# Optimization experiments

Measured on AMD Instinct MI355X. Metric: run time of the kernel, lower is better.

Reference implementation:

```python
import jax, jax.numpy as jnp
import numpy as np

B, T, D = 128, 197, 768          # batch, tokens, model dim
HEADS, HID_PER_HEAD = 12, 64
H = HEADS * HID_PER_HEAD         # lstm hidden size (== D by construction)


def _block_mask(in_per_head, hid_per_head, head_num):
    """Block-diagonal mask replicated over the 4 LSTM gates (i,f,g,o)."""
    Ht = hid_per_head * head_num
    Dt = in_per_head * head_num
    m = np.zeros((4 * Ht, Dt), np.float32)
    for h in range(head_num):
        for g in range(4):
            r0 = g * Ht + h * hid_per_head
            m[r0:r0 + hid_per_head, h * in_per_head:(h + 1) * in_per_head] = 1.0
    return jnp.asarray(m)


def setup_inputs() -> dict:
    key = jax.random.key(0)
    ks = jax.random.split(key, 16)
    s = 1.0 / np.sqrt(H)  # pytorch LSTM init scale
    u = lambda k, shape: jax.random.uniform(k, shape, jnp.float32, -s, s)
    mask_ih = _block_mask(D // HEADS, HID_PER_HEAD, HEADS)   # [4H, D]
    mask_hh = _block_mask(HID_PER_HEAD, HID_PER_HEAD, HEADS)  # [4H, H]
    inp = {
        "x": jax.random.normal(ks[0], (B, T, D), jnp.float32),
        "pre_w": u(ks[1], (D, D)),
        "pre_b": u(ks[2], (D,)),
        "w_ih_f": u(ks[3], (4 * H, D)) * mask_ih,
        "w_hh_f": u(ks[4], (4 * H, H)) * mask_hh,
        "b_ih_f": u(ks[5], (4 * H,)),
        "b_hh_f": u(ks[6], (4 * H,)),
        "w_ih_r": u(ks[7], (4 * H, D)) * mask_ih,
        "w_hh_r": u(ks[8], (4 * H, H)) * mask_hh,
        "b_ih_r": u(ks[9], (4 * H,)),
        "b_hh_r": u(ks[10], (4 * H,)),
        "proj_w": u(ks[11], (D, 2 * H)),
        "proj_b": u(ks[12], (D,)),
    }
    return inp


def _lstm_dir(x, w_ih, w_hh, b_ih, b_hh, reverse):
    # Precompute input contribution for all timesteps: [B,T,4H]
    xg = jnp.einsum('btd,gd->btg', x, w_ih) + b_ih + b_hh
    xs = jnp.swapaxes(xg, 0, 1)  # [T,B,4H]
    Bn = x.shape[0]

    def step(carry, gx):
        h, c = carry
        gates = gx + h @ w_hh.T
        i, f, g, o = jnp.split(gates, 4, axis=-1)  # pytorch gate order i,f,g,o
        i = jax.nn.sigmoid(i)
        f = jax.nn.sigmoid(f)
        g = jnp.tanh(g)
        o = jax.nn.sigmoid(o)
        c = f * c + i * g
        h = o * jnp.tanh(c)
        return (h, c), h

    init = (jnp.zeros((Bn, w_hh.shape[1]), x.dtype),
            jnp.zeros((Bn, w_hh.shape[1]), x.dtype))
    _, hs = jax.lax.scan(step, init, xs, reverse=reverse)  # outputs aligned to input order
    return jnp.swapaxes(hs, 0, 1)  # [B,T,H]


def reference(x, pre_w, pre_b, w_ih_f, w_hh_f, b_ih_f, b_hh_f,
              w_ih_r, w_hh_r, b_ih_r, b_hh_r, proj_w, proj_b):
    x = x @ pre_w.T + pre_b                      # pre_proj
    hf = _lstm_dir(x, w_ih_f, w_hh_f, b_ih_f, b_hh_f, reverse=False)
    hr = _lstm_dir(x, w_ih_r, w_hh_r, b_ih_r, b_hh_r, reverse=True)
    lstm_out = jnp.concatenate([hf, hr], axis=-1)  # [B,T,2H]
    return lstm_out @ proj_w.T + proj_b            # proj -> [B,T,D]
```

## Files before the change

kernel.cpp:

```cpp
#include <hip/hip_runtime.h>
#include <stdint.h>

#define DEV __device__ __forceinline__

typedef __attribute__((ext_vector_type(8))) short short8;
typedef __attribute__((ext_vector_type(4))) float floatx4;

#define BATCH 128
#define TT    197
#define DD    768
#define NH    12
#define NROWS (BATCH*TT)
#define G4H   3072

DEV uint16_t f2bf(float f) {
    union { float f; uint32_t u; } v; v.f = f;
    uint32_t r = (v.u + 0x7FFF + ((v.u >> 16) & 1)) >> 16;
    return (uint16_t)r;
}

DEV floatx4 mfma16(short8 a, short8 b, floatx4 c) {
    return __builtin_amdgcn_mfma_f32_16x16x32_bf16(a, b, c, 0, 0, 0);
}

DEV float sigf(float x)   { return __builtin_amdgcn_rcpf(1.0f + __expf(-x)); }
DEV float tanhf_(float x) { return 1.0f - 2.0f * __builtin_amdgcn_rcpf(1.0f + __expf(2.0f * x)); }

DEV void async16(const uint16_t* g, uint16_t* l) {
    __builtin_amdgcn_global_load_lds(
        (const __attribute__((address_space(1))) unsigned int*)g,
        (__attribute__((address_space(3))) unsigned int*)l,
        16, 0, 0);
}

__global__ void cvt_bf16(const float* __restrict__ src, uint16_t* __restrict__ dst, int n4) {
    int i = blockIdx.x * blockDim.x + threadIdx.x;
    int stride = gridDim.x * blockDim.x;
    for (; i < n4; i += stride) {
        float4 v = ((const float4*)src)[i];
        ushort4 o;
        o.x = f2bf(v.x); o.y = f2bf(v.y); o.z = f2bf(v.z); o.w = f2bf(v.w);
        ((ushort4*)dst)[i] = o;
    }
}

template<int STORE_BF16, int REMAP>
__global__ __launch_bounds__(256) void gemm128(
    const uint16_t* __restrict__ A,
    const uint16_t* __restrict__ Bw,
    const float*    __restrict__ bias,
    void*           __restrict__ C,
    int K, int Ntot)
{
    __shared__ __attribute__((aligned(16))) uint16_t As[128 * 32];
    __shared__ __attribute__((aligned(16))) uint16_t Bs[128 * 32];

    const int tid  = threadIdx.x;
    const int wv   = tid >> 6;
    const int lane = tid & 63;
    const int ln   = lane & 15;
    const int q    = lane >> 4;
    const int m0   = blockIdx.y * 128;
    const int n0   = blockIdx.x * 128;
    const int wm   = wv >> 1;
    const int wn   = wv & 1;

    floatx4 acc[4][4];
#pragma unroll
    for (int a = 0; a < 4; a++)
#pragma unroll
        for (int b = 0; b < 4; b++) acc[a][b] = (floatx4){0.f, 0.f, 0.f, 0.f};

    const uint16_t* gA0 = A  + (size_t)(m0 + (2*wv+0)*16 + ln) * K + q*8;
    const uint16_t* gA1 = A  + (size_t)(m0 + (2*wv+1)*16 + ln) * K + q*8;
    const uint16_t* gB0 = Bw + (size_t)(n0 + (2*wv+0)*16 + ln) * K + q*8;
    const uint16_t* gB1 = Bw + (size_t)(n0 + (2*wv+1)*16 + ln) * K + q*8;
    uint16_t* lA0 = &As[(2*wv+0) * 512];
    uint16_t* lA1 = &As[(2*wv+1) * 512];
    uint16_t* lB0 = &Bs[(2*wv+0) * 512];
    uint16_t* lB1 = &Bs[(2*wv+1) * 512];

    for (int k0 = 0; k0 < K; k0 += 32) {
        __syncthreads();
        async16(gA0 + k0, lA0);
        async16(gA1 + k0, lA1);
        async16(gB0 + k0, lB0);
        async16(gB1 + k0, lB1);
        __syncthreads();

        short8 af[4], bf[4];
#pragma unroll
        for (int mt = 0; mt < 4; mt++)
            af[mt] = *(const short8*)&As[(wm*4 + mt)*512 + lane*8];
#pragma unroll
        for (int nt = 0; nt < 4; nt++)
            bf[nt] = *(const short8*)&Bs[(wn*4 + nt)*512 + lane*8];
#pragma unroll
        for (int mt = 0; mt < 4; mt++)
#pragma unroll
            for (int nt = 0; nt < 4; nt++)
                acc[mt][nt] = mfma16(af[mt], bf[nt], acc[mt][nt]);
    }

#pragma unroll
    for (int mt = 0; mt < 4; mt++)
#pragma unroll
        for (int nt = 0; nt < 4; nt++) {
            int n = n0 + (wn*4 + nt)*16 + ln;
            float bv = bias[n];
#pragma unroll
            for (int r = 0; r < 4; r++) {
                int m = m0 + (wm*4 + mt)*16 + q*4 + r;
                float val = acc[mt][nt][r] + bv;
                int row;
                if (REMAP) { int b = m / 197; int t = m - b*197; row = t*128 + b; }
                else       { row = m; }
                if (STORE_BF16) ((uint16_t*)C)[(size_t)row * Ntot + n] = f2bf(val);
                else            ((float*)C)[(size_t)row * Ntot + n]    = val;
            }
        }
}

__global__ __launch_bounds__(256) void lstm_fused(
    const uint16_t* __restrict__ pre,
    const uint16_t* __restrict__ wih_f, const uint16_t* __restrict__ whh_f,
    const uint16_t* __restrict__ wih_r, const uint16_t* __restrict__ whh_r,
    const float* __restrict__ bih_f, const float* __restrict__ bhh_f,
    const float* __restrict__ bih_r, const float* __restrict__ bhh_r,
    uint16_t* __restrict__ hout)
{
    __shared__ __attribute__((aligned(16))) uint16_t hbuf[16][72];

    const int tid  = threadIdx.x;
    const int wv   = tid >> 6;
    const int lane = tid & 63;
    const int ln   = lane & 15;
    const int q    = lane >> 4;
    const int b0   = blockIdx.x * 16;
    const int head = blockIdx.y;
    const int dir  = blockIdx.z;
    const int ub   = wv * 16;

    const uint16_t* wih = dir ? wih_r : wih_f;
    const uint16_t* whh = dir ? whh_r : whh_f;
    const float*    bih = dir ? bih_r : bih_f;
    const float*    bhh = dir ? bhh_r : bhh_f;

    short8 aih[4][2], ahh[4][2];
#pragma unroll
    for (int t = 0; t < 4; t++) {
        size_t row = (size_t)(t*768 + head*64 + ub + ln);
#pragma unroll
        for (int s = 0; s < 2; s++) {
            aih[t][s] = *(const short8*)(wih + row*768 + head*64 + s*32 + q*8);
            ahh[t][s] = *(const short8*)(whh + row*768 + head*64 + s*32 + q*8);
        }
    }
    float biasv[4][4];
#pragma unroll
    for (int t = 0; t < 4; t++)
#pragma unroll
        for (int r = 0; r < 4; r++) {
            int row = t*768 + head*64 + ub + q*4 + r;
            biasv[t][r] = bih[row] + bhh[row];
        }

    for (int i = tid; i < 16*72; i += 256) ((uint16_t*)hbuf)[i] = 0;
    float c[4] = {0.f, 0.f, 0.f, 0.f};
    __syncthreads();

    const uint16_t* xbase = pre + head*64 + q*8;
    int t_cur = dir ? (TT - 1) : 0;
    const int tstep = dir ? -1 : 1;
    size_t xo = (size_t)(t_cur*128 + b0 + ln) * 768;
    short8 xv0 = *(const short8*)(xbase + xo);
    short8 xv1 = *(const short8*)(xbase + xo + 32);

    for (int step = 0; step < TT; step++) {
        short8 cx0 = xv0, cx1 = xv1;
        int t_next = t_cur + tstep;
        if (step + 1 < TT) {
            size_t xo2 = (size_t)(t_next*128 + b0 + ln) * 768;
            xv0 = *(const short8*)(xbase + xo2);
            xv1 = *(const short8*)(xbase + xo2 + 32);
        }
        short8 hb0 = *(const short8*)&hbuf[ln][0*32 + q*8];
        short8 hb1 = *(const short8*)&hbuf[ln][1*32 + q*8];

        floatx4 acc[4];
#pragma unroll
        for (int t = 0; t < 4; t++)
            acc[t] = (floatx4){biasv[t][0], biasv[t][1], biasv[t][2], biasv[t][3]};
#pragma unroll
        for (int t = 0; t < 4; t++) {
            acc[t] = mfma16(aih[t][0], cx0, acc[t]);
            acc[t] = mfma16(ahh[t][0], hb0, acc[t]);
            acc[t] = mfma16(aih[t][1], cx1, acc[t]);
            acc[t] = mfma16(ahh[t][1], hb1, acc[t]);
        }

        union { uint16_t s[4]; uint2 v; } hp;
#pragma unroll
        for (int r = 0; r < 4; r++) {
            float ig = sigf(acc[0][r]);
            float fg = sigf(acc[1][r]);
            float gg = tanhf_(acc[2][r]);
            float og = sigf(acc[3][r]);
            c[r] = fg * c[r] + ig * gg;
            float hv = og * tanhf_(c[r]);
            hp.s[r] = f2bf(hv);
        }

        __syncthreads();
        *(uint2*)&hbuf[ln][ub + q*4] = hp.v;
        __syncthreads();

        {
            int bl = tid >> 4;
            int dw = tid & 15;
            uint2 v = *(const uint2*)&hbuf[bl][dw*4];
            size_t off = ((size_t)(b0 + bl)*TT + t_cur) * 1536 + dir*768 + head*64 + dw*4;
            *(uint2*)(hout + off) = v;
        }
        t_cur = t_next;
    }
}

extern "C" void kernel_launch(void* const* d_in, const int* in_sizes, int n_in,
                              void* d_out, int out_size, void* d_ws, size_t ws_size,
                              hipStream_t stream) {
    (void)in_sizes; (void)n_in; (void)out_size; (void)ws_size;
    const float* x     = (const float*)d_in[0];
    const float* pre_w = (const float*)d_in[1];
    const float* pre_b = (const float*)d_in[2];
    const float* wihf  = (const float*)d_in[3];
    const float* whhf  = (const float*)d_in[4];
    const float* bihf  = (const float*)d_in[5];
    const float* bhhf  = (const float*)d_in[6];
    const float* wihr  = (const float*)d_in[7];
    const float* whhr  = (const float*)d_in[8];
    const float* bihr  = (const float*)d_in[9];
    const float* bhhr  = (const float*)d_in[10];
    const float* projw = (const float*)d_in[11];
    const float* projb = (const float*)d_in[12];
    float* out = (float*)d_out;

    uint16_t* W = (uint16_t*)d_ws;
    uint16_t* xb     = W; W += (size_t)NROWS * DD;
    uint16_t* bwpre  = W; W += (size_t)DD * DD;
    uint16_t* bwihf  = W; W += (size_t)G4H * DD;
    uint16_t* bwhhf  = W; W += (size_t)G4H * DD;
    uint16_t* bwihr  = W; W += (size_t)G4H * DD;
    uint16_t* bwhhr  = W; W += (size_t)G4H * DD;
    uint16_t* bwproj = W; W += (size_t)DD * 2 * DD;
    uint16_t* preb   = W; W += (size_t)NROWS * DD;
    uint16_t* houtb  = W; W += (size_t)NROWS * 2 * DD;

    auto cvt = [&](const float* s, uint16_t* d, size_t n) {
        int n4 = (int)(n / 4);
        int blocks = (n4 + 255) / 256; if (blocks > 4096) blocks = 4096;
        hipLaunchKernelGGL(cvt_bf16, dim3(blocks), dim3(256), 0, stream, s, d, n4);
    };
    cvt(x,     xb,     (size_t)NROWS * DD);
    cvt(pre_w, bwpre,  (size_t)DD * DD);
    cvt(wihf,  bwihf,  (size_t)G4H * DD);
    cvt(whhf,  bwhhf,  (size_t)G4H * DD);
    cvt(wihr,  bwihr,  (size_t)G4H * DD);
    cvt(whhr,  bwhhr,  (size_t)G4H * DD);
    cvt(projw, bwproj, (size_t)DD * 2 * DD);

    hipLaunchKernelGGL((gemm128<1, 1>), dim3(6, 197), dim3(256), 0, stream,
                       xb, bwpre, pre_b, (void*)preb, DD, DD);
    hipLaunchKernelGGL(lstm_fused, dim3(8, 12, 2), dim3(256), 0, stream,
                       preb, bwihf, bwhhf, bwihr, bwhhr,
                       bihf, bhhf, bihr, bhhr, houtb);
    hipLaunchKernelGGL((gemm128<0, 0>), dim3(6, 197), dim3(256), 0, stream,
                       houtb, bwproj, projb, (void*)out, 2 * DD, DD);
}
```

Measured before the change: 511.8 us.

## Fuse conversions, double-buffer LSTM h, head-major pre layout, swizzled GEMM grid

Merges the seven fp32-to-bf16 conversion launches into one multi-segment kernel. The GEMMs now load a 64-wide K slice per barrier pair and use a 1D grid with XCD-aware block swizzling. The pre-projection output is written in a [t][head][batch][64] layout so each LSTM step reads contiguous memory. The LSTM hidden state is double-buffered in LDS, which removes one barrier per recurrent step. Together these target launch overhead, barrier count on the serial recurrence and strided loads, at the cost of extra LDS and a more complex index mapping.

```diff
diff --git a/kernel.cpp b/kernel.cpp
--- a/kernel.cpp
+++ b/kernel.cpp
@@ -12,6 +12,8 @@
 #define NH    12
 #define NROWS (BATCH*TT)
 #define G4H   3072
+#define MT    197
+#define NT    6
 
 DEV uint16_t f2bf(float f) {
     union { float f; uint32_t u; } v; v.f = f;
@@ -33,18 +35,30 @@
         16, 0, 0);
 }
 
-__global__ void cvt_bf16(const float* __restrict__ src, uint16_t* __restrict__ dst, int n4) {
-    int i = blockIdx.x * blockDim.x + threadIdx.x;
+struct CvtArgs {
+    const float* src[7];
+    uint16_t*    dst[7];
+    int          n4[7];
+    int          nseg;
+};
+
+__global__ void cvt_multi(CvtArgs a) {
+    int tid = blockIdx.x * blockDim.x + threadIdx.x;
     int stride = gridDim.x * blockDim.x;
-    for (; i < n4; i += stride) {
-        float4 v = ((const float4*)src)[i];
-        ushort4 o;
-        o.x = f2bf(v.x); o.y = f2bf(v.y); o.z = f2bf(v.z); o.w = f2bf(v.w);
-        ((ushort4*)dst)[i] = o;
+    for (int s = 0; s < a.nseg; s++) {
+        const float4* src = (const float4*)a.src[s];
+        ushort4* dst = (ushort4*)a.dst[s];
+        int n4 = a.n4[s];
+        for (int i = tid; i < n4; i += stride) {
+            float4 v = src[i];
+            ushort4 o;
+            o.x = f2bf(v.x); o.y = f2bf(v.y); o.z = f2bf(v.z); o.w = f2bf(v.w);
+            dst[i] = o;
+        }
     }
 }
 
-template<int STORE_BF16, int REMAP>
+template<int STORE_BF16, int LAYOUT>
 __global__ __launch_bounds__(256) void gemm128(
     const uint16_t* __restrict__ A,
     const uint16_t* __restrict__ Bw,
@@ -52,16 +66,23 @@
     void*           __restrict__ C,
     int K, int Ntot)
 {
-    __shared__ __attribute__((aligned(16))) uint16_t As[128 * 32];
-    __shared__ __attribute__((aligned(16))) uint16_t Bs[128 * 32];
+    __shared__ __attribute__((aligned(16))) uint16_t As[2][8 * 512];
+    __shared__ __attribute__((aligned(16))) uint16_t Bs[2][8 * 512];
+
+    const int bid = blockIdx.x;
+    const int c   = bid & 7;
+    const int j   = bid >> 3;
+    const int mt_ = c + 8 * (j / NT);
+    const int nt_ = j % NT;
+    if (mt_ >= MT) return;
+    const int m0 = mt_ * 128;
+    const int n0 = nt_ * 128;
 
     const int tid  = threadIdx.x;
     const int wv   = tid >> 6;
     const int lane = tid & 63;
     const int ln   = lane & 15;
     const int q    = lane >> 4;
-    const int m0   = blockIdx.y * 128;
-    const int n0   = blockIdx.x * 128;
     const int wm   = wv >> 1;
     const int wn   = wv & 1;
 
@@ -75,31 +96,38 @@
     const uint16_t* gA1 = A  + (size_t)(m0 + (2*wv+1)*16 + ln) * K + q*8;
     const uint16_t* gB0 = Bw + (size_t)(n0 + (2*wv+0)*16 + ln) * K + q*8;
     const uint16_t* gB1 = Bw + (size_t)(n0 + (2*wv+1)*16 + ln) * K + q*8;
-    uint16_t* lA0 = &As[(2*wv+0) * 512];
-    uint16_t* lA1 = &As[(2*wv+1) * 512];
-    uint16_t* lB0 = &Bs[(2*wv+0) * 512];
-    uint16_t* lB1 = &Bs[(2*wv+1) * 512];
-
-    for (int k0 = 0; k0 < K; k0 += 32) {
+    uint16_t* lA0h0 = &As[0][(2*wv+0)*512]; uint16_t* lA0h1 = &As[1][(2*wv+0)*512];
+    uint16_t* lA1h0 = &As[0][(2*wv+1)*512]; uint16_t* lA1h1 = &As[1][(2*wv+1)*512];
+    uint16_t* lB0h0 = &Bs[0][(2*wv+0)*512]; uint16_t* lB0h1 = &Bs[1][(2*wv+0)*512];
+    uint16_t* lB1h0 = &Bs[0][(2*wv+1)*512]; uint16_t* lB1h1 = &Bs[1][(2*wv+1)*512];
+
+    for (int k0 = 0; k0 < K; k0 += 64) {
         __syncthreads();
-        async16(gA0 + k0, lA0);
-        async16(gA1 + k0, lA1);
-        async16(gB0 + k0, lB0);
-        async16(gB1 + k0, lB1);
+        async16(gA0 + k0,      lA0h0);
+        async16(gA0 + k0 + 32, lA0h1);
+        async16(gA1 + k0,      lA1h0);
+        async16(gA1 + k0 + 32, lA1h1);
+        async16(gB0 + k0,      lB0h0);
+        async16(gB0 + k0 + 32, lB0h1);
+        async16(gB1 + k0,      lB1h0);
+        async16(gB1 + k0 + 32, lB1h1);
         __syncthreads();
 
-        short8 af[4], bf[4];
-#pragma unroll
-        for (int mt = 0; mt < 4; mt++)
-            af[mt] = *(const short8*)&As[(wm*4 + mt)*512 + lane*8];
-#pragma unroll
-        for (int nt = 0; nt < 4; nt++)
-            bf[nt] = *(const short8*)&Bs[(wn*4 + nt)*512 + lane*8];
-#pragma unroll
-        for (int mt = 0; mt < 4; mt++)
+#pragma unroll
+        for (int h = 0; h < 2; h++) {
+            short8 af[4], bf[4];
+#pragma unroll
+            for (int mt = 0; mt < 4; mt++)
+                af[mt] = *(const short8*)&As[h][(wm*4 + mt)*512 + lane*8];
 #pragma unroll
             for (int nt = 0; nt < 4; nt++)
-                acc[mt][nt] = mfma16(af[mt], bf[nt], acc[mt][nt]);
+                bf[nt] = *(const short8*)&Bs[h][(wn*4 + nt)*512 + lane*8];
+#pragma unroll
+            for (int mt = 0; mt < 4; mt++)
+#pragma unroll
+                for (int nt = 0; nt < 4; nt++)
+                    acc[mt][nt] = mfma16(af[mt], bf[nt], acc[mt][nt]);
+        }
     }
 
 #pragma unroll
@@ -112,11 +140,16 @@
             for (int r = 0; r < 4; r++) {
                 int m = m0 + (wm*4 + mt)*16 + q*4 + r;
                 float val = acc[mt][nt][r] + bv;
-                int row;
-                if (REMAP) { int b = m / 197; int t = m - b*197; row = t*128 + b; }
-                else       { row = m; }
-                if (STORE_BF16) ((uint16_t*)C)[(size_t)row * Ntot + n] = f2bf(val);
-                else            ((float*)C)[(size_t)row * Ntot + n]    = val;
+                if (LAYOUT == 1) {
+                    int b = m / 197; int t = m - b*197;
+                    int head = n >> 6; int d = n & 63;
+                    size_t off = ((size_t)(t*NH + head)*BATCH + b)*64 + d;
+                    ((uint16_t*)C)[off] = f2bf(val);
+                } else {
+                    size_t off = (size_t)m * Ntot + n;
+                    if (STORE_BF16) ((uint16_t*)C)[off] = f2bf(val);
+                    else            ((float*)C)[off]    = val;
+                }
             }
         }
 }
@@ -129,7 +162,7 @@
     const float* __restrict__ bih_r, const float* __restrict__ bhh_r,
     uint16_t* __restrict__ hout)
 {
-    __shared__ __attribute__((aligned(16))) uint16_t hbuf[16][72];
+    __shared__ __attribute__((aligned(16))) uint16_t hbuf[2][16][72];
 
     const int tid  = threadIdx.x;
     const int wv   = tid >> 6;
@@ -165,14 +198,14 @@
             biasv[t][r] = bih[row] + bhh[row];
         }
 
-    for (int i = tid; i < 16*72; i += 256) ((uint16_t*)hbuf)[i] = 0;
+    for (int i = tid; i < 2*16*72; i += 256) ((uint16_t*)hbuf)[i] = 0;
     float c[4] = {0.f, 0.f, 0.f, 0.f};
     __syncthreads();
 
-    const uint16_t* xbase = pre + head*64 + q*8;
+    const uint16_t* xbase = pre + (size_t)head*BATCH*64 + (size_t)(b0 + ln)*64 + q*8;
     int t_cur = dir ? (TT - 1) : 0;
     const int tstep = dir ? -1 : 1;
-    size_t xo = (size_t)(t_cur*128 + b0 + ln) * 768;
+    size_t xo = (size_t)t_cur * NH * BATCH * 64;
     short8 xv0 = *(const short8*)(xbase + xo);
     short8 xv1 = *(const short8*)(xbase + xo + 32);
 
@@ -180,12 +213,14 @@
         short8 cx0 = xv0, cx1 = xv1;
         int t_next = t_cur + tstep;
         if (step + 1 < TT) {
-            size_t xo2 = (size_t)(t_next*128 + b0 + ln) * 768;
+            size_t xo2 = (size_t)t_next * NH * BATCH * 64;
             xv0 = *(const short8*)(xbase + xo2);
             xv1 = *(const short8*)(xbase + xo2 + 32);
         }
-        short8 hb0 = *(const short8*)&hbuf[ln][0*32 + q*8];
-        short8 hb1 = *(const short8*)&hbuf[ln][1*32 + q*8];
+        const int pb = (step + 1) & 1;
+        const int cb = step & 1;
+        short8 hb0 = *(const short8*)&hbuf[pb][ln][0*32 + q*8];
+        short8 hb1 = *(const short8*)&hbuf[pb][ln][1*32 + q*8];
 
         floatx4 acc[4];
 #pragma unroll
@@ -211,14 +246,13 @@
             hp.s[r] = f2bf(hv);
         }
 
-        __syncthreads();
-        *(uint2*)&hbuf[ln][ub + q*4] = hp.v;
+        *(uint2*)&hbuf[cb][ln][ub + q*4] = hp.v;
         __syncthreads();
 
         {
             int bl = tid >> 4;
             int dw = tid & 15;
-            uint2 v = *(const uint2*)&hbuf[bl][dw*4];
+            uint2 v = *(const uint2*)&hbuf[cb][bl][dw*4];
             size_t off = ((size_t)(b0 + bl)*TT + t_cur) * 1536 + dir*768 + head*64 + dw*4;
             *(uint2*)(hout + off) = v;
         }
@@ -256,24 +290,25 @@
     uint16_t* preb   = W; W += (size_t)NROWS * DD;
     uint16_t* houtb  = W; W += (size_t)NROWS * 2 * DD;
 
-    auto cvt = [&](const float* s, uint16_t* d, size_t n) {
-        int n4 = (int)(n / 4);
-        int blocks = (n4 + 255) / 256; if (blocks > 4096) blocks = 4096;
-        hipLaunchKernelGGL(cvt_bf16, dim3(blocks), dim3(256), 0, stream, s, d, n4);
-    };
-    cvt(x,     xb,     (size_t)NROWS * DD);
-    cvt(pre_w, bwpre,  (size_t)DD * DD);
-    cvt(wihf,  bwihf,  (size_t)G4H * DD);
-    cvt(whhf,  bwhhf,  (size_t)G4H * DD);
-    cvt(wihr,  bwihr,  (size_t)G4H * DD);
-    cvt(whhr,  bwhhr,  (size_t)G4H * DD);
-    cvt(projw, bwproj, (size_t)DD * 2 * DD);
-
-    hipLaunchKernelGGL((gemm128<1, 1>), dim3(6, 197), dim3(256), 0, stream,
+    CvtArgs ca;
+    ca.src[0] = x;     ca.dst[0] = xb;     ca.n4[0] = (int)((size_t)NROWS * DD / 4);
+    ca.src[1] = pre_w; ca.dst[1] = bwpre;  ca.n4[1] = DD * DD / 4;
+    ca.src[2] = wihf;  ca.dst[2] = bwihf;  ca.n4[2] = G4H * DD / 4;
+    ca.src[3] = whhf;  ca.dst[3] = bwhhf;  ca.n4[3] = G4H * DD / 4;
+    ca.src[4] = wihr;  ca.dst[4] = bwihr;  ca.n4[4] = G4H * DD / 4;
+    ca.src[5] = whhr;  ca.dst[5] = bwhhr;  ca.n4[5] = G4H * DD / 4;
+    ca.src[6] = projw; ca.dst[6] = bwproj; ca.n4[6] = DD * 2 * DD / 4;
+    ca.nseg = 7;
+    hipLaunchKernelGGL(cvt_multi, dim3(1024), dim3(256), 0, stream, ca);
+
+    const int RPX = (MT + 7) / 8;
+    const int GBLK = 8 * RPX * NT;
+
+    hipLaunchKernelGGL((gemm128<1, 1>), dim3(GBLK), dim3(256), 0, stream,
                        xb, bwpre, pre_b, (void*)preb, DD, DD);
     hipLaunchKernelGGL(lstm_fused, dim3(8, 12, 2), dim3(256), 0, stream,
                        preb, bwihf, bwhhf, bwihr, bwhhr,
                        bihf, bhhf, bihr, bhhr, houtb);
-    hipLaunchKernelGGL((gemm128<0, 0>), dim3(6, 197), dim3(256), 0, stream,
+    hipLaunchKernelGGL((gemm128<0, 0>), dim3(GBLK), dim3(256), 0, stream,
                        houtb, bwproj, projb, (void*)out, 2 * DD, DD);
 }
```

Result: no change. 516.0 us (+0.8%).
